# Performance work log

Measured on AMD Instinct MI355X. Metric: run time of the kernel, lower is better.

Reference implementation:

```python
import jax, jax.numpy as jnp
import numpy as np

DIM = 256
HEADS = 8

def conv1x1(x, W, b):
    # x: [b,c,h,w], W: [o,c], b: [o]
    return jnp.einsum('oc,bchw->bohw', W, x) + b[None, :, None, None]

def setup_inputs() -> dict:
    key = jax.random.key(0)
    ks = jax.random.split(key, 16)
    B, C, H, Wd = 8, DIM, 96, 96
    s = 1.0 / np.sqrt(C)
    inp = {
        'x': jax.random.normal(ks[0], (B, C, H, Wd), jnp.float32),
        'y': jax.random.normal(ks[1], (B, C, H, Wd), jnp.float32),
        'z': jax.random.normal(ks[2], (B, C, H, Wd), jnp.float32),
        'W_qr': jax.random.normal(ks[3], (C // 2, C), jnp.float32) * s,
        'b_qr': jnp.zeros((C // 2,), jnp.float32),
        'W_qd': jax.random.normal(ks[4], (C // 2, C), jnp.float32) * s,
        'b_qd': jnp.zeros((C // 2,), jnp.float32),
        'W_kf': jax.random.normal(ks[5], (C, C), jnp.float32) * s,
        'b_kf': jnp.zeros((C,), jnp.float32),
        'W_vf': jax.random.normal(ks[6], (C, C), jnp.float32) * s,
        'b_vf': jnp.zeros((C,), jnp.float32),
        'W_cat': jax.random.normal(ks[7], (C, C), jnp.float32) * s,
        'b_cat': jnp.zeros((C,), jnp.float32),
        'W_proj': jax.random.normal(ks[8], (C, C), jnp.float32) * s,
        'b_proj': jnp.zeros((C,), jnp.float32),
        'temperature': jnp.ones((HEADS, 1, 1), jnp.float32),
    }
    return inp

def reference(x, y, z, W_qr, b_qr, W_qd, b_qd, W_kf, b_kf, W_vf, b_vf,
              W_cat, b_cat, W_proj, b_proj, temperature):
    b, c, h, w = x.shape
    hw = h * w
    ch = c // HEADS  # channels per head

    q_r = conv1x1(x, W_qr, b_qr)
    q_d = conv1x1(y, W_qd, b_qd)
    k_f = conv1x1(z, W_kf, b_kf)
    v_f = conv1x1(z, W_vf, b_vf)
    q = conv1x1(jnp.concatenate([q_r, q_d], axis=1), W_cat, b_cat)

    def to_heads(t):  # [b, head*ch, h, w] -> [b, head, ch, hw]
        return t.reshape(b, HEADS, ch, hw)

    q = to_heads(q)
    k = to_heads(k_f)
    v = to_heads(v_f)

    # L2-normalize along spatial axis (eps=1e-12 as in F.normalize)
    q = q / jnp.maximum(jnp.linalg.norm(q, axis=-1, keepdims=True), 1e-12)
    k = k / jnp.maximum(jnp.linalg.norm(k, axis=-1, keepdims=True), 1e-12)

    # channel attention: [b,head,ch,ch]
    attn = jnp.einsum('bhcn,bhdn->bhcd', q, k) * temperature[None]
    attn = jax.nn.softmax(attn, axis=-1)
    out = jnp.einsum('bhcd,bhdn->bhcn', attn, v)  # [b,head,ch,hw]
    out = out.reshape(b, c, h, w)
    return conv1x1(out, W_proj, b_proj) + z
```

## Files before the change

kernel.cpp:

```cpp
#include <hip/hip_runtime.h>

#define HW 9216
#define CDIM 256
#define NBATCH 8
#define NHEADS 8
#define GCH 9

typedef __bf16 bf16x8 __attribute__((ext_vector_type(8)));
typedef float f32x4 __attribute__((ext_vector_type(4)));
typedef float f32x2 __attribute__((ext_vector_type(2)));
typedef float f32x16 __attribute__((ext_vector_type(16)));
typedef unsigned short us2v __attribute__((ext_vector_type(2)));
typedef unsigned short us4v __attribute__((ext_vector_type(4)));
typedef unsigned short us8v __attribute__((ext_vector_type(8)));
typedef unsigned int u32x4 __attribute__((ext_vector_type(4)));

__device__ inline unsigned short f2bf(float f) {
    unsigned int u = __builtin_bit_cast(unsigned int, f);
    u = (u + 0x7FFF + ((u >> 16) & 1)) >> 16;
    return (unsigned short)u;
}
__device__ inline float bf2f(unsigned short s) {
    unsigned int u = ((unsigned int)s) << 16;
    return __builtin_bit_cast(float, u);
}
__device__ inline unsigned int pk2(float a, float b) {
    return (unsigned int)f2bf(a) | ((unsigned int)f2bf(b) << 16);
}
__device__ inline void stx(float* p, float v) { *p = v; }
__device__ inline void stx(unsigned short* p, float v) { *p = f2bf(v); }

__global__ void fuse_wq(const float* __restrict__ W_cat, const float* __restrict__ W_qr,
                        const float* __restrict__ W_qd, const float* __restrict__ b_qr,
                        const float* __restrict__ b_qd, const float* __restrict__ b_cat,
                        unsigned short* __restrict__ Wq, float* __restrict__ bq) {
    int o = blockIdx.x;
    int c = threadIdx.x;
    float ax = 0.f, ay = 0.f;
    for (int i = 0; i < 128; ++i) {
        ax += W_cat[o * 256 + i] * W_qr[i * 256 + c];
        ay += W_cat[o * 256 + 128 + i] * W_qd[i * 256 + c];
    }
    Wq[o * 512 + c] = f2bf(ax);
    Wq[o * 512 + 256 + c] = f2bf(ay);
    if (c == 0) {
        float s = b_cat[o];
        for (int i = 0; i < 128; ++i)
            s += W_cat[o * 256 + i] * b_qr[i] + W_cat[o * 256 + 128 + i] * b_qd[i];
        bq[o] = s;
    }
}

__global__ void cvt_w(const float* __restrict__ a, const float* __restrict__ b,
                      unsigned short* __restrict__ oa, unsigned short* __restrict__ ob) {
    int i = blockIdx.x * 256 + threadIdx.x;
    oa[i] = f2bf(a[i]);
    ob[i] = f2bf(b[i]);
}

template <int BN, bool DUAL, typename TX, typename TOut>
__global__ __launch_bounds__(256, 2) void gemm2(
    const unsigned short* __restrict__ A0, const unsigned short* __restrict__ A1,
    int a_bs, int Ktot,
    const TX* __restrict__ X0, const TX* __restrict__ X1,
    const float* __restrict__ bias0, const float* __restrict__ bias1,
    const float* __restrict__ resid, TOut* __restrict__ O0, TOut* __restrict__ O1) {
    constexpr int NJ = BN / 32;
    constexpr int NLD = (BN == 128) ? 4 : 2;
    constexpr int BUFB = 8 * BN * 16;

    const int b = blockIdx.z;
    const int n0 = blockIdx.x * BN;
    const int m0 = blockIdx.y * 128;
    const int tid = threadIdx.x;
    const int lane = tid & 63;
    const int wid = tid >> 6;
    const int wm = (wid >> 1) * 64;
    const int wn = (wid & 1) * (BN / 2);
    const int l15 = lane & 15;
    const int quad = lane >> 4;

    __shared__ __align__(16) char Bs[2][BUFB];

    const unsigned short* Ab0 = A0 + (size_t)b * a_bs;
    const unsigned short* Ab1 = DUAL ? A1 : nullptr;
    const TX* Xb0 = X0 + (size_t)b * CDIM * HW;
    const TX* Xb1 = X1 ? X1 + (size_t)b * CDIM * HW : nullptr;

    const int sn = (tid & 31) * NLD;
    const int so = (tid >> 5) * 8;

    f32x4 acc0[4][NJ] = {};
    f32x4 acc1[DUAL ? 4 : 1][NJ] = {};
    float f[8][NLD];

    auto LOADS = [&](int kg) {
        const TX* Xp = (Xb1 && kg >= 256) ? Xb1 : Xb0;
        const int kr = kg & 255;
#pragma unroll
        for (int r = 0; r < 8; ++r) {
            const TX* p = Xp + (size_t)(kr + so + r) * HW + n0 + sn;
            if constexpr (sizeof(TX) == 4) {
                if constexpr (NLD == 4) {
                    f32x4 v = *(const f32x4*)p;
#pragma unroll
                    for (int j = 0; j < 4; ++j) f[r][j] = v[j];
                } else {
                    f32x2 v = *(const f32x2*)p;
                    f[r][0] = v[0]; f[r][1] = v[1];
                }
            } else {
                if constexpr (NLD == 4) {
                    us4v v = *(const us4v*)p;
#pragma unroll
                    for (int j = 0; j < 4; ++j) f[r][j] = bf2f(v[j]);
                } else {
                    us2v v = *(const us2v*)p;
                    f[r][0] = bf2f(v[0]); f[r][1] = bf2f(v[1]);
                }
            }
        }
    };

    auto PKW = [&](int buf) {
        char* base = &Bs[buf][0];
#pragma unroll
        for (int j = 0; j < NLD; ++j) {
            int n = sn + j;
            u32x4 w;
            w[0] = pk2(f[0][j], f[1][j]);
            w[1] = pk2(f[2][j], f[3][j]);
            w[2] = pk2(f[4][j], f[5][j]);
            w[3] = pk2(f[6][j], f[7][j]);
            *(u32x4*)(base + ((((so >> 3) * BN + n) * 16) ^ ((n & 0x38) << 1))) = w;
        }
    };

    auto COMPUTE = [&](int buf, int k0) {
        const char* base = &Bs[buf][0];
#pragma unroll
        for (int kk = 0; kk < 64; kk += 32) {
            bf16x8 bfr[NJ];
#pragma unroll
            for (int nj = 0; nj < NJ; ++nj) {
                int n = wn + nj * 16 + l15;
                bfr[nj] = *(const bf16x8*)(base +
                    (((((kk >> 3) + quad) * BN + n) * 16) ^ ((n & 0x38) << 1)));
            }
            bf16x8 af[4];
#pragma unroll
            for (int mi = 0; mi < 4; ++mi)
                af[mi] = *(const bf16x8*)(Ab0 + (size_t)(m0 + wm + mi * 16 + l15) * Ktot +
                                          k0 + kk + quad * 8);
#pragma unroll
            for (int mi = 0; mi < 4; ++mi)
#pragma unroll
                for (int nj = 0; nj < NJ; ++nj)
                    acc0[mi][nj] = __builtin_amdgcn_mfma_f32_16x16x32_bf16(af[mi], bfr[nj],
                                                                           acc0[mi][nj], 0, 0, 0);
            if constexpr (DUAL) {
#pragma unroll
                for (int mi = 0; mi < 4; ++mi)
                    af[mi] = *(const bf16x8*)(Ab1 + (size_t)(m0 + wm + mi * 16 + l15) * Ktot +
                                              k0 + kk + quad * 8);
#pragma unroll
                for (int mi = 0; mi < 4; ++mi)
#pragma unroll
                    for (int nj = 0; nj < NJ; ++nj)
                        acc1[mi][nj] = __builtin_amdgcn_mfma_f32_16x16x32_bf16(af[mi], bfr[nj],
                                                                               acc1[mi][nj], 0, 0, 0);
            }
        }
    };

    const int nt = Ktot >> 6;
    LOADS(0);
    PKW(0);
    __syncthreads();
    for (int t = 0; t < nt - 1; ++t) {
        LOADS((t + 1) << 6);
        __builtin_amdgcn_sched_barrier(0);
        COMPUTE(t & 1, t << 6);
        PKW((t + 1) & 1);
        __syncthreads();
    }
    COMPUTE((nt - 1) & 1, (nt - 1) << 6);

#pragma unroll
    for (int mi = 0; mi < 4; ++mi) {
#pragma unroll
        for (int r = 0; r < 4; ++r) {
            int m = m0 + wm + mi * 16 + quad * 4 + r;
            float bv = bias0[m];
#pragma unroll
            for (int nj = 0; nj < NJ; ++nj) {
                int n = n0 + wn + nj * 16 + l15;
                size_t off = ((size_t)b * CDIM + m) * HW + n;
                float v = acc0[mi][nj][r] + bv;
                if (resid) v += resid[off];
                stx(&O0[off], v);
            }
        }
    }
    if constexpr (DUAL) {
#pragma unroll
        for (int mi = 0; mi < 4; ++mi) {
#pragma unroll
            for (int r = 0; r < 4; ++r) {
                int m = m0 + wm + mi * 16 + quad * 4 + r;
                float bv = bias1[m];
#pragma unroll
                for (int nj = 0; nj < NJ; ++nj) {
                    int n = n0 + wn + nj * 16 + l15;
                    size_t off = ((size_t)b * CDIM + m) * HW + n;
                    stx(&O1[off], acc1[mi][nj][r] + bv);
                }
            }
        }
    }
}

__global__ __launch_bounds__(256) void gram_mfma(
    const unsigned short* __restrict__ q, const unsigned short* __restrict__ k,
    float* __restrict__ Gp, float* __restrict__ sqp, float* __restrict__ skp) {
    const int ch = blockIdx.x;
    const int bh = blockIdx.y;
    const int t = threadIdx.x;
    const int lane = t & 63, w = t >> 6;
    const int row = lane & 31, half = lane >> 5;

    const size_t rb = ((size_t)bh * 32 + row) * HW + ch * 1024 + w * 256 + half * 8;
    const unsigned short* qp = q + rb;
    const unsigned short* kp = k + rb;

    f32x16 acc = {};
    float sq = 0.f, sk = 0.f;
#pragma unroll
    for (int n = 0; n < 256; n += 16) {
        us8v rq = *(const us8v*)(qp + n);
        us8v rk = *(const us8v*)(kp + n);
        bf16x8 aq = __builtin_bit_cast(bf16x8, rq);
        bf16x8 ak = __builtin_bit_cast(bf16x8, rk);
        acc = __builtin_amdgcn_mfma_f32_32x32x16_bf16(aq, ak, acc, 0, 0, 0);
#pragma unroll
        for (int j = 0; j < 8; ++j) {
            float fq = bf2f(rq[j]);
            float fk = bf2f(rk[j]);
            sq += fq * fq;
            sk += fk * fk;
        }
    }
    sq += __shfl_xor(sq, 32, 64);
    sk += __shfl_xor(sk, 32, 64);

    __shared__ float gs[4][1024];
    __shared__ float sqs[4][32];
    __shared__ float sks[4][32];
    if (half == 0) { sqs[w][row] = sq; sks[w][row] = sk; }
#pragma unroll
    for (int r = 0; r < 16; ++r) {
        int cr = (r & 3) + 8 * (r >> 2) + 4 * half;
        gs[w][cr * 32 + row] = acc[r];
    }
    __syncthreads();

    float* Gpo = Gp + ((size_t)ch * 64 + bh) * 1024;
#pragma unroll
    for (int j = 0; j < 4; ++j) {
        int idx = j * 256 + t;
        Gpo[idx] = gs[0][idx] + gs[1][idx] + gs[2][idx] + gs[3][idx];
    }
    if (t < 32)
        sqp[((size_t)ch * 64 + bh) * 32 + t] = sqs[0][t] + sqs[1][t] + sqs[2][t] + sqs[3][t];
    else if (t < 64) {
        int c = t - 32;
        skp[((size_t)ch * 64 + bh) * 32 + c] = sks[0][c] + sks[1][c] + sks[2][c] + sks[3][c];
    }
}

__global__ __launch_bounds__(1024) void softmax_kernel(
    const float* __restrict__ Gp, const float* __restrict__ sqp,
    const float* __restrict__ skp, const float* __restrict__ temp,
    float* __restrict__ A) {
    int bh = blockIdx.x;
    int h = bh & 7;
    int c = threadIdx.y, d = threadIdx.x;
    float g = 0.f, qq = 0.f, kk = 0.f;
#pragma unroll
    for (int ch = 0; ch < GCH; ++ch) {
        g += Gp[((size_t)ch * 64 + bh) * 1024 + c * 32 + d];
        qq += sqp[((size_t)ch * 64 + bh) * 32 + c];
        kk += skp[((size_t)ch * 64 + bh) * 32 + d];
    }
    float nq = fmaxf(sqrtf(qq), 1e-12f);
    float nk = fmaxf(sqrtf(kk), 1e-12f);
    float v = g / (nq * nk) * temp[h];
    float m = v;
    for (int s = 16; s > 0; s >>= 1) m = fmaxf(m, __shfl_xor(m, s, 32));
    float e = __expf(v - m);
    float sum = e;
    for (int s = 16; s > 0; s >>= 1) sum += __shfl_xor(sum, s, 32);
    A[(size_t)(bh * 32 + c) * 32 + d] = e / sum;
}

__global__ __launch_bounds__(256) void build_m(const float* __restrict__ W_proj,
                                               const float* __restrict__ A,
                                               unsigned short* __restrict__ M) {
    int o = blockIdx.x;
    int b = blockIdx.y;
    int t = threadIdx.x;
    int h = t >> 5, d = t & 31;
    const float* Ab = A + (size_t)(b * 8 + h) * 32 * 32;
    float acc = 0.f;
    for (int c = 0; c < 32; ++c)
        acc += W_proj[o * 256 + h * 32 + c] * Ab[c * 32 + d];
    M[((size_t)b * 256 + o) * 256 + t] = f2bf(acc);
}

extern "C" void kernel_launch(void* const* d_in, const int* in_sizes, int n_in,
                              void* d_out, int out_size, void* d_ws, size_t ws_size,
                              hipStream_t stream) {
    const float* x = (const float*)d_in[0];
    const float* y = (const float*)d_in[1];
    const float* z = (const float*)d_in[2];
    const float* W_qr = (const float*)d_in[3];
    const float* b_qr = (const float*)d_in[4];
    const float* W_qd = (const float*)d_in[5];
    const float* b_qd = (const float*)d_in[6];
    const float* W_kf = (const float*)d_in[7];
    const float* b_kf = (const float*)d_in[8];
    const float* W_vf = (const float*)d_in[9];
    const float* b_vf = (const float*)d_in[10];
    const float* W_cat = (const float*)d_in[11];
    const float* b_cat = (const float*)d_in[12];
    const float* W_proj = (const float*)d_in[13];
    const float* b_proj = (const float*)d_in[14];
    const float* temp = (const float*)d_in[15];
    float* out = (float*)d_out;

    char* ws = (char*)d_ws;
    const size_t NT = (size_t)NBATCH * CDIM * HW;
    unsigned short* qb = (unsigned short*)ws;
    unsigned short* kb = qb + NT;
    unsigned short* vb = kb + NT;
    char* p = (char*)(vb + NT);
    unsigned short* Wq = (unsigned short*)p;  p += 256 * 512 * 2;
    unsigned short* Wk = (unsigned short*)p;  p += 256 * 256 * 2;
    unsigned short* Wv = (unsigned short*)p;  p += 256 * 256 * 2;
    float* bq  = (float*)p;                   p += 1024;
    float* Gp  = (float*)p;                   p += (size_t)GCH * 64 * 1024 * 4;
    float* sqp = (float*)p;                   p += GCH * 64 * 32 * 4;
    float* skp = (float*)p;                   p += GCH * 64 * 32 * 4;
    float* Aat = (float*)p;                   p += 64 * 32 * 32 * 4;
    unsigned short* Mb = (unsigned short*)p;  p += (size_t)8 * 256 * 256 * 2;

    fuse_wq<<<256, 256, 0, stream>>>(W_cat, W_qr, W_qd, b_qr, b_qd, b_cat, Wq, bq);
    cvt_w<<<256, 256, 0, stream>>>(W_kf, W_vf, Wk, Wv);

    gemm2<128, false, float, unsigned short><<<dim3(HW / 128, 2, NBATCH), 256, 0, stream>>>(
        Wq, nullptr, 0, 512, x, y, bq, nullptr, nullptr, qb, nullptr);
    gemm2<64, true, float, unsigned short><<<dim3(HW / 64, 2, NBATCH), 256, 0, stream>>>(
        Wk, Wv, 0, 256, z, nullptr, b_kf, b_vf, nullptr, kb, vb);

    gram_mfma<<<dim3(GCH, 64), 256, 0, stream>>>(qb, kb, Gp, sqp, skp);
    softmax_kernel<<<64, dim3(32, 32), 0, stream>>>(Gp, sqp, skp, temp, Aat);
    build_m<<<dim3(256, 8), 256, 0, stream>>>(W_proj, Aat, Mb);

    gemm2<128, false, unsigned short, float><<<dim3(HW / 128, 2, NBATCH), 256, 0, stream>>>(
        Mb, nullptr, 256 * 256, 256, vb, nullptr, b_proj, nullptr, z, out, nullptr);
}
```

Measured before the change: 517.6 us.

## Restructure GEMM into 512-thread 64x256 tiles with LDS-staged weights and swizzled grid

Replaces the 128xBN GEMM kernel with a 512-thread kernel that computes 64 output rows by 256 columns per block, using a K step of 32. Weight tiles are now staged through shared memory instead of being read directly from global memory inside the MFMA loop. A linear 1D grid is remapped so that consecutive blocks interleave across XCD groups. The new B-tile layout swaps its swizzle for an even/odd column split. The aim is better occupancy, more reuse of the input activations across all output rows, and fewer scattered global weight loads. In exchange it adds twice as many K iterations and barriers, and risks LDS bank conflicts from the new layout.

```diff
diff --git a/kernel.cpp b/kernel.cpp
--- a/kernel.cpp
+++ b/kernel.cpp
@@ -58,144 +58,145 @@
     ob[i] = f2bf(b[i]);
 }
 
-template <int BN, bool DUAL, typename TX, typename TOut>
-__global__ __launch_bounds__(256, 2) void gemm2(
+template <bool DUAL, typename TX, typename TOut>
+__global__ __launch_bounds__(512, 4) void gemm3(
     const unsigned short* __restrict__ A0, const unsigned short* __restrict__ A1,
     int a_bs, int Ktot,
     const TX* __restrict__ X0, const TX* __restrict__ X1,
     const float* __restrict__ bias0, const float* __restrict__ bias1,
     const float* __restrict__ resid, TOut* __restrict__ O0, TOut* __restrict__ O1) {
-    constexpr int NJ = BN / 32;
-    constexpr int NLD = (BN == 128) ? 4 : 2;
-    constexpr int BUFB = 8 * BN * 16;
-
-    const int b = blockIdx.z;
-    const int n0 = blockIdx.x * BN;
-    const int m0 = blockIdx.y * 128;
+    constexpr int ROWSA = DUAL ? 128 : 64;
+    constexpr int ABYTES = 4 * ROWSA * 16;
+    constexpr int BBYTES = 4 * 256 * 16;
+
+    __shared__ __align__(16) char As[2][ABYTES];
+    __shared__ __align__(16) char Bs[2][BBYTES];
+
+    const int h = blockIdx.x;
+    const int lid = (h & 7) * 144 + (h >> 3);
+    const int by = lid & 3;
+    const int bx = (lid >> 2) % 36;
+    const int bz = (lid >> 2) / 36;
+    const int m0 = by * 64;
+    const int n0 = bx * 256;
+
     const int tid = threadIdx.x;
     const int lane = tid & 63;
     const int wid = tid >> 6;
-    const int wm = (wid >> 1) * 64;
-    const int wn = (wid & 1) * (BN / 2);
     const int l15 = lane & 15;
     const int quad = lane >> 4;
-
-    __shared__ __align__(16) char Bs[2][BUFB];
-
-    const unsigned short* Ab0 = A0 + (size_t)b * a_bs;
+    const int wn = wid * 32;
+
+    const unsigned short* Ab0 = A0 + (size_t)bz * a_bs;
     const unsigned short* Ab1 = DUAL ? A1 : nullptr;
-    const TX* Xb0 = X0 + (size_t)b * CDIM * HW;
-    const TX* Xb1 = X1 ? X1 + (size_t)b * CDIM * HW : nullptr;
-
-    const int sn = (tid & 31) * NLD;
-    const int so = (tid >> 5) * 8;
-
-    f32x4 acc0[4][NJ] = {};
-    f32x4 acc1[DUAL ? 4 : 1][NJ] = {};
-    float f[8][NLD];
-
-    auto LOADS = [&](int kg) {
+    const TX* Xb0 = X0 + (size_t)bz * CDIM * HW;
+    const TX* Xb1 = X1 ? X1 + (size_t)bz * CDIM * HW : nullptr;
+
+    const int bc = (tid & 127) * 2;
+    const int brg = tid >> 7;
+    const int aq8 = DUAL ? (tid >> 7) : (tid >> 6);
+    const int arow = DUAL ? (tid & 127) : (tid & 63);
+    const int amat = DUAL ? (arow >> 6) : 0;
+    const int amrow = arow & 63;
+
+    f32x4 acc0[4][2] = {};
+    f32x4 acc1[DUAL ? 4 : 1][2] = {};
+    float f[8][2];
+    us8v areg = {};
+
+    auto LOADG = [&](int kg) {
         const TX* Xp = (Xb1 && kg >= 256) ? Xb1 : Xb0;
         const int kr = kg & 255;
 #pragma unroll
-        for (int r = 0; r < 8; ++r) {
-            const TX* p = Xp + (size_t)(kr + so + r) * HW + n0 + sn;
+        for (int j = 0; j < 8; ++j) {
+            const TX* p = Xp + (size_t)(kr + brg * 8 + j) * HW + n0 + bc;
             if constexpr (sizeof(TX) == 4) {
-                if constexpr (NLD == 4) {
-                    f32x4 v = *(const f32x4*)p;
-#pragma unroll
-                    for (int j = 0; j < 4; ++j) f[r][j] = v[j];
-                } else {
-                    f32x2 v = *(const f32x2*)p;
-                    f[r][0] = v[0]; f[r][1] = v[1];
-                }
+                f32x2 v = *(const f32x2*)p;
+                f[j][0] = v[0]; f[j][1] = v[1];
             } else {
-                if constexpr (NLD == 4) {
-                    us4v v = *(const us4v*)p;
-#pragma unroll
-                    for (int j = 0; j < 4; ++j) f[r][j] = bf2f(v[j]);
-                } else {
-                    us2v v = *(const us2v*)p;
-                    f[r][0] = bf2f(v[0]); f[r][1] = bf2f(v[1]);
-                }
+                us2v v = *(const us2v*)p;
+                f[j][0] = bf2f(v[0]); f[j][1] = bf2f(v[1]);
             }
         }
+        if (DUAL || tid < 256) {
+            const unsigned short* Aw = amat ? Ab1 : Ab0;
+            areg = *(const us8v*)(Aw + (size_t)(m0 + amrow) * Ktot + kg + aq8 * 8);
+        }
     };
 
-    auto PKW = [&](int buf) {
-        char* base = &Bs[buf][0];
-#pragma unroll
-        for (int j = 0; j < NLD; ++j) {
-            int n = sn + j;
+    auto STORE = [&](int buf) {
+        char* bb = &Bs[buf][0];
+#pragma unroll
+        for (int j2 = 0; j2 < 2; ++j2) {
+            int n = bc + j2;
             u32x4 w;
-            w[0] = pk2(f[0][j], f[1][j]);
-            w[1] = pk2(f[2][j], f[3][j]);
-            w[2] = pk2(f[4][j], f[5][j]);
-            w[3] = pk2(f[6][j], f[7][j]);
-            *(u32x4*)(base + ((((so >> 3) * BN + n) * 16) ^ ((n & 0x38) << 1))) = w;
-        }
+            w[0] = pk2(f[0][j2], f[1][j2]);
+            w[1] = pk2(f[2][j2], f[3][j2]);
+            w[2] = pk2(f[4][j2], f[5][j2]);
+            w[3] = pk2(f[6][j2], f[7][j2]);
+            int slot = brg * 256 + ((n >> 1) | ((n & 1) << 7));
+            *(u32x4*)(bb + slot * 16) = w;
+        }
+        if (DUAL || tid < 256)
+            *(us8v*)(&As[buf][0] + (size_t)tid * 16) = areg;
     };
 
-    auto COMPUTE = [&](int buf, int k0) {
-        const char* base = &Bs[buf][0];
-#pragma unroll
-        for (int kk = 0; kk < 64; kk += 32) {
-            bf16x8 bfr[NJ];
-#pragma unroll
-            for (int nj = 0; nj < NJ; ++nj) {
-                int n = wn + nj * 16 + l15;
-                bfr[nj] = *(const bf16x8*)(base +
-                    (((((kk >> 3) + quad) * BN + n) * 16) ^ ((n & 0x38) << 1)));
-            }
-            bf16x8 af[4];
+    auto COMPUTE = [&](int buf) {
+        const char* bb = &Bs[buf][0];
+        const char* ab = &As[buf][0];
+        bf16x8 bfr[2];
+#pragma unroll
+        for (int nj = 0; nj < 2; ++nj) {
+            int n = wn + nj * 16 + l15;
+            int slot = quad * 256 + ((n >> 1) | ((n & 1) << 7));
+            bfr[nj] = *(const bf16x8*)(bb + slot * 16);
+        }
+        bf16x8 af[4];
+#pragma unroll
+        for (int mi = 0; mi < 4; ++mi)
+            af[mi] = *(const bf16x8*)(ab + (quad * ROWSA + mi * 16 + l15) * 16);
+#pragma unroll
+        for (int mi = 0; mi < 4; ++mi)
+#pragma unroll
+            for (int nj = 0; nj < 2; ++nj)
+                acc0[mi][nj] = __builtin_amdgcn_mfma_f32_16x16x32_bf16(af[mi], bfr[nj],
+                                                                       acc0[mi][nj], 0, 0, 0);
+        if constexpr (DUAL) {
 #pragma unroll
             for (int mi = 0; mi < 4; ++mi)
-                af[mi] = *(const bf16x8*)(Ab0 + (size_t)(m0 + wm + mi * 16 + l15) * Ktot +
-                                          k0 + kk + quad * 8);
+                af[mi] = *(const bf16x8*)(ab + (quad * ROWSA + 64 + mi * 16 + l15) * 16);
 #pragma unroll
             for (int mi = 0; mi < 4; ++mi)
 #pragma unroll
-                for (int nj = 0; nj < NJ; ++nj)
-                    acc0[mi][nj] = __builtin_amdgcn_mfma_f32_16x16x32_bf16(af[mi], bfr[nj],
-                                                                           acc0[mi][nj], 0, 0, 0);
-            if constexpr (DUAL) {
-#pragma unroll
-                for (int mi = 0; mi < 4; ++mi)
-                    af[mi] = *(const bf16x8*)(Ab1 + (size_t)(m0 + wm + mi * 16 + l15) * Ktot +
-                                              k0 + kk + quad * 8);
-#pragma unroll
-                for (int mi = 0; mi < 4; ++mi)
-#pragma unroll
-                    for (int nj = 0; nj < NJ; ++nj)
-                        acc1[mi][nj] = __builtin_amdgcn_mfma_f32_16x16x32_bf16(af[mi], bfr[nj],
-                                                                               acc1[mi][nj], 0, 0, 0);
-            }
+                for (int nj = 0; nj < 2; ++nj)
+                    acc1[mi][nj] = __builtin_amdgcn_mfma_f32_16x16x32_bf16(af[mi], bfr[nj],
+                                                                           acc1[mi][nj], 0, 0, 0);
         }
     };
 
-    const int nt = Ktot >> 6;
-    LOADS(0);
-    PKW(0);
+    const int nt = Ktot >> 5;
+    LOADG(0);
+    STORE(0);
     __syncthreads();
     for (int t = 0; t < nt - 1; ++t) {
-        LOADS((t + 1) << 6);
+        LOADG((t + 1) << 5);
         __builtin_amdgcn_sched_barrier(0);
-        COMPUTE(t & 1, t << 6);
-        PKW((t + 1) & 1);
+        COMPUTE(t & 1);
+        STORE((t + 1) & 1);
         __syncthreads();
     }
-    COMPUTE((nt - 1) & 1, (nt - 1) << 6);
+    COMPUTE((nt - 1) & 1);
 
 #pragma unroll
     for (int mi = 0; mi < 4; ++mi) {
 #pragma unroll
         for (int r = 0; r < 4; ++r) {
-            int m = m0 + wm + mi * 16 + quad * 4 + r;
+            int m = m0 + mi * 16 + quad * 4 + r;
             float bv = bias0[m];
 #pragma unroll
-            for (int nj = 0; nj < NJ; ++nj) {
+            for (int nj = 0; nj < 2; ++nj) {
                 int n = n0 + wn + nj * 16 + l15;
-                size_t off = ((size_t)b * CDIM + m) * HW + n;
+                size_t off = ((size_t)bz * CDIM + m) * HW + n;
                 float v = acc0[mi][nj][r] + bv;
                 if (resid) v += resid[off];
                 stx(&O0[off], v);
@@ -207,12 +208,12 @@
         for (int mi = 0; mi < 4; ++mi) {
 #pragma unroll
             for (int r = 0; r < 4; ++r) {
-                int m = m0 + wm + mi * 16 + quad * 4 + r;
+                int m = m0 + mi * 16 + quad * 4 + r;
                 float bv = bias1[m];
 #pragma unroll
-                for (int nj = 0; nj < NJ; ++nj) {
+                for (int nj = 0; nj < 2; ++nj) {
                     int n = n0 + wn + nj * 16 + l15;
-                    size_t off = ((size_t)b * CDIM + m) * HW + n;
+                    size_t off = ((size_t)bz * CDIM + m) * HW + n;
                     stx(&O1[off], acc1[mi][nj][r] + bv);
                 }
             }
@@ -357,15 +358,15 @@
     fuse_wq<<<256, 256, 0, stream>>>(W_cat, W_qr, W_qd, b_qr, b_qd, b_cat, Wq, bq);
     cvt_w<<<256, 256, 0, stream>>>(W_kf, W_vf, Wk, Wv);
 
-    gemm2<128, false, float, unsigned short><<<dim3(HW / 128, 2, NBATCH), 256, 0, stream>>>(
+    gemm3<false, float, unsigned short><<<1152, 512, 0, stream>>>(
         Wq, nullptr, 0, 512, x, y, bq, nullptr, nullptr, qb, nullptr);
-    gemm2<64, true, float, unsigned short><<<dim3(HW / 64, 2, NBATCH), 256, 0, stream>>>(
+    gemm3<true, float, unsigned short><<<1152, 512, 0, stream>>>(
         Wk, Wv, 0, 256, z, nullptr, b_kf, b_vf, nullptr, kb, vb);
 
     gram_mfma<<<dim3(GCH, 64), 256, 0, stream>>>(qb, kb, Gp, sqp, skp);
     softmax_kernel<<<64, dim3(32, 32), 0, stream>>>(Gp, sqp, skp, temp, Aat);
     build_m<<<dim3(256, 8), 256, 0, stream>>>(W_proj, Aat, Mb);
 
-    gemm2<128, false, unsigned short, float><<<dim3(HW / 128, 2, NBATCH), 256, 0, stream>>>(
+    gemm3<false, unsigned short, float><<<1152, 512, 0, stream>>>(
         Mb, nullptr, 256 * 256, 256, vb, nullptr, b_proj, nullptr, z, out, nullptr);
 }
```

Measured after the change: 492.5 us. -4.9%, faster.
